# Performance work log

Measured on AMD Instinct MI355X. Metric: run time of the kernel, lower is better.

Reference implementation:

```python
import jax, jax.numpy as jnp
import numpy as np

TEMPERATURE = 0.5

def setup_inputs() -> dict:
    key = jax.random.key(0)
    k1, k2 = jax.random.split(key)
    B, D = 4096, 256
    embeddings_i = jax.random.normal(k1, (B, D), dtype=jnp.float32)
    embeddings_j = jax.random.normal(k2, (B, D), dtype=jnp.float32)
    return {"embeddings_i": embeddings_i, "embeddings_j": embeddings_j}

def reference(embeddings_i, embeddings_j):
    B = embeddings_i.shape[0]
    N = 2 * B
    # concat and L2-normalize rows
    z = jnp.concatenate([embeddings_i, embeddings_j], axis=0)  # [2B, D]
    z = z / jnp.linalg.norm(z, axis=1, keepdims=True)
    # pairwise cosine similarity / temperature: [2B, 2B]
    sim = jnp.matmul(z, z.T) / TEMPERATURE
    # mask self-similarity on the diagonal with -inf
    diag = jnp.arange(N)
    sim = sim.at[diag, diag].set(-jnp.inf)
    # positive pair index for each row: i<->i+B
    labels = jnp.concatenate([jnp.arange(B, N), jnp.arange(B)], axis=0)
    # softmax cross-entropy (mean over rows)
    logp = jax.nn.log_softmax(sim, axis=1)
    loss = -jnp.mean(jnp.take_along_axis(logp, labels[:, None], axis=1))
    return loss
```

## Files before the change

kernel.cpp:

```cpp
#include <hip/hip_runtime.h>
#include <hip/hip_bf16.h>

#define N_TOT 8192
#define BHALF 4096
#define DIM   256
#define INV_T 2.0f

typedef __attribute__((ext_vector_type(8))) short bf16x8;
typedef __attribute__((ext_vector_type(4))) float f32x4;

__device__ __forceinline__ float b2f(unsigned short u) {
  union { unsigned u; float f; } cv; cv.u = ((unsigned)u) << 16; return cv.f;
}
__device__ __forceinline__ unsigned short f2b(float f) {
  union { float f; unsigned u; } cv; cv.f = f;
  unsigned u = cv.u;
  u += 0x7FFFu + ((u >> 16) & 1u);
  return (unsigned short)(u >> 16);
}

__global__ __launch_bounds__(256) void normalize_kernel(
    const float* __restrict__ ei, const float* __restrict__ ej,
    unsigned short* __restrict__ zn) {
  const int wave = threadIdx.x >> 6, lane = threadIdx.x & 63;
  const int row = blockIdx.x * 4 + wave;
  const float* src = (row < BHALF) ? (ei + (size_t)row * DIM)
                                   : (ej + (size_t)(row - BHALF) * DIM);
  float4 v = *reinterpret_cast<const float4*>(src + lane * 4);
  float ss = v.x * v.x + v.y * v.y + v.z * v.z + v.w * v.w;
#pragma unroll
  for (int off = 32; off; off >>= 1) ss += __shfl_xor(ss, off, 64);
  float inv = rsqrtf(ss);
  ushort4 o;
  o.x = f2b(v.x * inv); o.y = f2b(v.y * inv);
  o.z = f2b(v.z * inv); o.w = f2b(v.w * inv);
  *reinterpret_cast<ushort4*>(zn + (size_t)row * DIM + lane * 4) = o;
}

__global__ __launch_bounds__(256) void posdot_kernel(
    const unsigned short* __restrict__ zn, float* __restrict__ p) {
  const int wave = threadIdx.x >> 6, lane = threadIdx.x & 63;
  const int i = blockIdx.x * 4 + wave;
  const ushort4 a = *reinterpret_cast<const ushort4*>(zn + (size_t)i * DIM + lane * 4);
  const ushort4 b = *reinterpret_cast<const ushort4*>(zn + (size_t)(i + BHALF) * DIM + lane * 4);
  float s = b2f(a.x) * b2f(b.x) + b2f(a.y) * b2f(b.y) +
            b2f(a.z) * b2f(b.z) + b2f(a.w) * b2f(b.w);
#pragma unroll
  for (int off = 32; off; off >>= 1) s += __shfl_xor(s, off, 64);
  if (lane == 0) p[i] = s * INV_T;
}

__global__ __launch_bounds__(256) void simexp_kernel(
    const unsigned short* __restrict__ zn, float* __restrict__ S) {
  __shared__ __align__(16) unsigned short As[128 * 64];
  __shared__ __align__(16) unsigned short Bs[128 * 64];
  const int tid = threadIdx.x;
  const int wave = tid >> 6, lane = tid & 63;
  const int bi = blockIdx.x, bj = blockIdx.y;
  const int wr = wave >> 1, wc = wave & 1;

  f32x4 acc[4][4] = {};

  const int fragrow_a = wr * 64 + (lane & 15);
  const int fragrow_b = wc * 64 + (lane & 15);
  const int kcolb = (lane >> 4) * 16;

  const unsigned short* gA = zn + (size_t)bi * 128 * DIM;
  const unsigned short* gB = zn + (size_t)bj * 128 * DIM;

  const int lrow  = lane >> 3;
  const int lslot = (lane & 7) * 16;

  for (int kt = 0; kt < 4; ++kt) {
#pragma unroll
    for (int r = 0; r < 4; ++r) {
      const int c = wave * 4 + r;
      const int row = c * 8 + lrow;
      const int colb = lslot ^ ((row & 7) << 4);
      const unsigned short* sA = gA + (size_t)row * DIM + kt * 64 + (colb >> 1);
      const unsigned short* sB = gB + (size_t)row * DIM + kt * 64 + (colb >> 1);
      __builtin_amdgcn_global_load_lds(
          (const __attribute__((address_space(1))) void*)sA,
          (__attribute__((address_space(3))) void*)(As + c * 512), 16, 0, 0);
      __builtin_amdgcn_global_load_lds(
          (const __attribute__((address_space(1))) void*)sB,
          (__attribute__((address_space(3))) void*)(Bs + c * 512), 16, 0, 0);
    }
    __syncthreads();

#pragma unroll
    for (int ks = 0; ks < 2; ++ks) {
      bf16x8 af[4], bfr[4];
#pragma unroll
      for (int m = 0; m < 4; ++m) {
        const int row = fragrow_a + m * 16;
        const int byt = row * 128 + ((ks * 64 + kcolb) ^ ((row & 7) << 4));
        af[m] = *reinterpret_cast<const bf16x8*>(
            reinterpret_cast<const char*>(As) + byt);
      }
#pragma unroll
      for (int n = 0; n < 4; ++n) {
        const int row = fragrow_b + n * 16;
        const int byt = row * 128 + ((ks * 64 + kcolb) ^ ((row & 7) << 4));
        bfr[n] = *reinterpret_cast<const bf16x8*>(
            reinterpret_cast<const char*>(Bs) + byt);
      }
#pragma unroll
      for (int m = 0; m < 4; ++m)
#pragma unroll
        for (int n = 0; n < 4; ++n)
          acc[m][n] = __builtin_amdgcn_mfma_f32_16x16x32_bf16(
              af[m], bfr[n], acc[m][n], 0, 0, 0);
    }
    __syncthreads();
  }

  const int grow0 = bi * 128 + wr * 64 + (lane >> 4) * 4;
  const int gcol0 = bj * 128 + wc * 64 + (lane & 15);
#pragma unroll
  for (int m = 0; m < 4; ++m) {
    float rs[4] = {0.f, 0.f, 0.f, 0.f};
#pragma unroll
    for (int n = 0; n < 4; ++n) {
      const int gc = gcol0 + n * 16;
#pragma unroll
      for (int r = 0; r < 4; ++r) {
        const int gr = grow0 + m * 16 + r;
        float v = __expf(acc[m][n][r] * INV_T);
        v = (gr == gc) ? 0.f : v;
        rs[r] += v;
      }
    }
#pragma unroll
    for (int off = 1; off < 16; off <<= 1) {
#pragma unroll
      for (int r = 0; r < 4; ++r) rs[r] += __shfl_xor(rs[r], off, 64);
    }
    if ((lane & 15) == 0) {
#pragma unroll
      for (int r = 0; r < 4; ++r)
        atomicAdd(&S[grow0 + m * 16 + r], rs[r]);
    }
  }
}

__global__ __launch_bounds__(256) void finalize_kernel(
    const float* __restrict__ S, const float* __restrict__ p,
    float* __restrict__ out) {
  float acc = 0.f;
  for (int i = threadIdx.x; i < N_TOT; i += 256) {
    const int pi = (i < BHALF) ? i : (i - BHALF);
    acc += logf(S[i]) - p[pi];
  }
#pragma unroll
  for (int off = 32; off; off >>= 1) acc += __shfl_xor(acc, off, 64);
  __shared__ float red[4];
  const int wave = threadIdx.x >> 6, lane = threadIdx.x & 63;
  if (lane == 0) red[wave] = acc;
  __syncthreads();
  if (threadIdx.x == 0)
    out[0] = (red[0] + red[1] + red[2] + red[3]) / (float)N_TOT;
}

extern "C" void kernel_launch(void* const* d_in, const int* in_sizes, int n_in,
                              void* d_out, int out_size, void* d_ws, size_t ws_size,
                              hipStream_t stream) {
  const float* ei = (const float*)d_in[0];
  const float* ej = (const float*)d_in[1];
  float* out = (float*)d_out;

  char* ws = (char*)d_ws;
  unsigned short* zn = (unsigned short*)ws;
  float* S = (float*)(ws + (size_t)N_TOT * DIM * 2);
  float* p = (float*)(ws + (size_t)N_TOT * DIM * 2 + N_TOT * 4);

  (void)hipMemsetAsync(S, 0, N_TOT * sizeof(float), stream);
  normalize_kernel<<<N_TOT / 4, 256, 0, stream>>>(ei, ej, zn);
  posdot_kernel<<<BHALF / 4, 256, 0, stream>>>(zn, p);
  dim3 grid(N_TOT / 128, N_TOT / 128);
  simexp_kernel<<<grid, 256, 0, stream>>>(zn, S);
  finalize_kernel<<<1, 256, 0, stream>>>(S, p, out);
}
```

Baseline: 120.1 us.

## Exploit symmetry of similarity matrix, fuse posdot and memset into other kernels

The similarity GEMM now computes only upper-triangular 128x128 tiles (2080 instead of 4096 blocks). Each off-diagonal tile adds its exp row sums and column sums to S, so the mirrored tile is never computed. The positive-pair logits are taken from the accumulators of the b==a+32 tiles, which removes the posdot kernel. The memset is folded into the normalize kernel. The trade-offs are more atomics per block, a small loop that maps the linear block index to a triangle position, and some extra epilogue work.

```diff
diff --git a/kernel.cpp b/kernel.cpp
--- a/kernel.cpp
+++ b/kernel.cpp
@@ -21,7 +21,8 @@
 
 __global__ __launch_bounds__(256) void normalize_kernel(
     const float* __restrict__ ei, const float* __restrict__ ej,
-    unsigned short* __restrict__ zn) {
+    unsigned short* __restrict__ zn, float* __restrict__ S) {
+  if (threadIdx.x < 4) S[blockIdx.x * 4 + threadIdx.x] = 0.f;
   const int wave = threadIdx.x >> 6, lane = threadIdx.x & 63;
   const int row = blockIdx.x * 4 + wave;
   const float* src = (row < BHALF) ? (ei + (size_t)row * DIM)
@@ -37,26 +38,21 @@
   *reinterpret_cast<ushort4*>(zn + (size_t)row * DIM + lane * 4) = o;
 }
 
-__global__ __launch_bounds__(256) void posdot_kernel(
-    const unsigned short* __restrict__ zn, float* __restrict__ p) {
-  const int wave = threadIdx.x >> 6, lane = threadIdx.x & 63;
-  const int i = blockIdx.x * 4 + wave;
-  const ushort4 a = *reinterpret_cast<const ushort4*>(zn + (size_t)i * DIM + lane * 4);
-  const ushort4 b = *reinterpret_cast<const ushort4*>(zn + (size_t)(i + BHALF) * DIM + lane * 4);
-  float s = b2f(a.x) * b2f(b.x) + b2f(a.y) * b2f(b.y) +
-            b2f(a.z) * b2f(b.z) + b2f(a.w) * b2f(b.w);
-#pragma unroll
-  for (int off = 32; off; off >>= 1) s += __shfl_xor(s, off, 64);
-  if (lane == 0) p[i] = s * INV_T;
-}
-
 __global__ __launch_bounds__(256) void simexp_kernel(
-    const unsigned short* __restrict__ zn, float* __restrict__ S) {
+    const unsigned short* __restrict__ zn, float* __restrict__ S,
+    float* __restrict__ p) {
   __shared__ __align__(16) unsigned short As[128 * 64];
   __shared__ __align__(16) unsigned short Bs[128 * 64];
   const int tid = threadIdx.x;
   const int wave = tid >> 6, lane = tid & 63;
-  const int bi = blockIdx.x, bj = blockIdx.y;
+
+  int t = blockIdx.x;
+  int a = 0;
+  while ((a + 1) * 64 - ((a + 1) * a) / 2 <= t) ++a;
+  const int b = a + (t - (a * 64 - (a * (a - 1)) / 2));
+  const bool offdiag = (b != a);
+  const bool need_p = (b == a + 32);
+
   const int wr = wave >> 1, wc = wave & 1;
 
   f32x4 acc[4][4] = {};
@@ -65,8 +61,8 @@
   const int fragrow_b = wc * 64 + (lane & 15);
   const int kcolb = (lane >> 4) * 16;
 
-  const unsigned short* gA = zn + (size_t)bi * 128 * DIM;
-  const unsigned short* gB = zn + (size_t)bj * 128 * DIM;
+  const unsigned short* gA = zn + (size_t)a * 128 * DIM;
+  const unsigned short* gB = zn + (size_t)b * 128 * DIM;
 
   const int lrow  = lane >> 3;
   const int lslot = (lane & 7) * 16;
@@ -115,22 +111,30 @@
     __syncthreads();
   }
 
-  const int grow0 = bi * 128 + wr * 64 + (lane >> 4) * 4;
-  const int gcol0 = bj * 128 + wc * 64 + (lane & 15);
+  const int grow0 = a * 128 + wr * 64 + (lane >> 4) * 4;
+  const int gcol0 = b * 128 + wc * 64 + (lane & 15);
+
 #pragma unroll
-  for (int m = 0; m < 4; ++m) {
-    float rs[4] = {0.f, 0.f, 0.f, 0.f};
+  for (int m = 0; m < 4; ++m)
 #pragma unroll
-    for (int n = 0; n < 4; ++n) {
-      const int gc = gcol0 + n * 16;
+    for (int n = 0; n < 4; ++n)
 #pragma unroll
       for (int r = 0; r < 4; ++r) {
         const int gr = grow0 + m * 16 + r;
-        float v = __expf(acc[m][n][r] * INV_T);
-        v = (gr == gc) ? 0.f : v;
-        rs[r] += v;
+        const int gc = gcol0 + n * 16;
+        const float raw = acc[m][n][r];
+        if (need_p && gc == gr + BHALF) p[gr] = raw * INV_T;
+        float v = __expf(raw * INV_T);
+        if (gr == gc) v = 0.f;
+        acc[m][n][r] = v;
       }
-    }
+
+#pragma unroll
+  for (int m = 0; m < 4; ++m) {
+    float rs[4];
+#pragma unroll
+    for (int r = 0; r < 4; ++r)
+      rs[r] = acc[m][0][r] + acc[m][1][r] + acc[m][2][r] + acc[m][3][r];
 #pragma unroll
     for (int off = 1; off < 16; off <<= 1) {
 #pragma unroll
@@ -140,6 +144,20 @@
 #pragma unroll
       for (int r = 0; r < 4; ++r)
         atomicAdd(&S[grow0 + m * 16 + r], rs[r]);
+    }
+  }
+
+  if (offdiag) {
+#pragma unroll
+    for (int n = 0; n < 4; ++n) {
+      float cs = 0.f;
+#pragma unroll
+      for (int m = 0; m < 4; ++m)
+#pragma unroll
+        for (int r = 0; r < 4; ++r) cs += acc[m][n][r];
+      cs += __shfl_xor(cs, 16, 64);
+      cs += __shfl_xor(cs, 32, 64);
+      if (lane < 16) atomicAdd(&S[gcol0 + n * 16], cs);
     }
   }
 }
@@ -174,10 +192,7 @@
   float* S = (float*)(ws + (size_t)N_TOT * DIM * 2);
   float* p = (float*)(ws + (size_t)N_TOT * DIM * 2 + N_TOT * 4);
 
-  (void)hipMemsetAsync(S, 0, N_TOT * sizeof(float), stream);
-  normalize_kernel<<<N_TOT / 4, 256, 0, stream>>>(ei, ej, zn);
-  posdot_kernel<<<BHALF / 4, 256, 0, stream>>>(zn, p);
-  dim3 grid(N_TOT / 128, N_TOT / 128);
-  simexp_kernel<<<grid, 256, 0, stream>>>(zn, S);
+  normalize_kernel<<<N_TOT / 4, 256, 0, stream>>>(ei, ej, zn, S);
+  simexp_kernel<<<(64 * 65) / 2, 256, 0, stream>>>(zn, S, p);
   finalize_kernel<<<1, 256, 0, stream>>>(S, p, out);
 }
```

After: 119.9 us. Within noise of the previous version (-0.2%).
